# Kernel tuning notes

Hardware: AMD Instinct MI355X
Metric: run time of the kernel (lower is better)

The kernel has to match this reference:

```python
import jax, jax.numpy as jnp
import numpy as np

N = 50000          # nodes
E = 1250000        # edges (avg degree 25)
EMBED = 64
HIDS = [64, 64, 64]
EDGE_DIM = 7       # 1 + 6
VOCAB = 5 ** 8     # 390625
NEG_SLOPE = 0.01   # F.leaky_relu default


def setup_inputs() -> dict:
    key = jax.random.key(0)
    ks = jax.random.split(key, 14)
    L = len(HIDS)
    x = jax.random.randint(ks[0], (N,), 0, VOCAB)
    edge_index = jax.random.randint(ks[1], (2, E), 0, N)
    edge_attr = jax.random.normal(ks[2], (E, EDGE_DIM), dtype=jnp.float32)
    emb = jax.random.normal(ks[3], (VOCAB, EMBED), dtype=jnp.float32) * 0.02
    # all layers have in = out = 64, so params are stacked along layer axis
    lin1_w = jax.random.normal(ks[4], (L, EMBED + EDGE_DIM, HIDS[0]), dtype=jnp.float32) * 0.1
    att_l = jax.random.normal(ks[5], (L, HIDS[0]), dtype=jnp.float32) * 0.1
    att_r = jax.random.normal(ks[6], (L, EMBED), dtype=jnp.float32) * 0.1
    lin2_w = jax.random.normal(ks[7], (L, HIDS[0], HIDS[0]), dtype=jnp.float32) * 0.1
    gbias = jax.random.normal(ks[8], (L, HIDS[0]), dtype=jnp.float32) * 0.01
    d_cat = int(np.sum(HIDS)) + EMBED  # 256
    fc1_w = jax.random.normal(ks[9], (d_cat, 20), dtype=jnp.float32) * 0.05
    fc1_b = jax.random.normal(ks[10], (20,), dtype=jnp.float32) * 0.01
    fc2_w = jax.random.normal(ks[11], (20, 1), dtype=jnp.float32) * 0.1
    fc2_b = jax.random.normal(ks[12], (1,), dtype=jnp.float32) * 0.01
    return {"x": x, "edge_index": edge_index, "edge_attr": edge_attr, "emb": emb,
            "lin1_w": lin1_w, "att_l": att_l, "att_r": att_r, "lin2_w": lin2_w,
            "gbias": gbias, "fc1_w": fc1_w, "fc1_b": fc1_b, "fc2_w": fc2_w, "fc2_b": fc2_b}


def _gate_conv(h, src, dst, edge_attr, w1, al, ar, w2, b):
    # message from source j -> target i; attention softmax over edges sharing a target
    xj = jnp.concatenate([h[src], edge_attr], axis=-1)            # [E, in+7]
    xj = jax.nn.leaky_relu(xj @ w1, NEG_SLOPE)                    # [E, out]
    alpha = jax.nn.leaky_relu(jnp.sum(xj * al, -1) + jnp.sum(h[dst] * ar, -1), NEG_SLOPE)
    amax = jax.ops.segment_max(alpha, dst, num_segments=N)        # [N]
    ea = jnp.exp(alpha - amax[dst])                               # [E]
    denom = jax.ops.segment_sum(ea, dst, num_segments=N)          # [N]
    a = ea / (denom[dst] + 1e-16)
    msg = (xj @ w2) * a[:, None]                                  # [E, out]
    return jax.ops.segment_sum(msg, dst, num_segments=N) + b      # [N, out]


def reference(x, edge_index, edge_attr, emb, lin1_w, att_l, att_r, lin2_w,
              gbias, fc1_w, fc1_b, fc2_w, fc2_b):
    src, dst = edge_index[0], edge_index[1]
    h = emb[x]                                                    # [N, EMBED]
    feats = [h]
    for l in range(len(HIDS)):
        h = jax.nn.relu(_gate_conv(h, src, dst, edge_attr,
                                   lin1_w[l], att_l[l], att_r[l], lin2_w[l], gbias[l]))
        feats.append(h)
    hcat = jnp.concatenate(feats, axis=-1)                        # [N, 256]
    z = jax.nn.relu(hcat @ fc1_w + fc1_b)
    out = jax.nn.sigmoid(z @ fc2_w + fc2_b)
    return out.squeeze(-1)                                        # [N]
```

## Files before the change

kernel.cpp:

```cpp
#include <hip/hip_runtime.h>
#include <math.h>

#define NEG 0.01f

typedef _Float16 f16;
typedef f16 h2 __attribute__((ext_vector_type(2)));

__device__ __forceinline__ float lrelu(float x) { return x > 0.f ? x : NEG * x; }

__device__ __forceinline__ h2 lrelu2(h2 x) {
    h2 y = x * (f16)0.01f;
    return __builtin_elementwise_max(x, y);
}

__device__ __forceinline__ float q16_allsum(float v) {
    int x;
    x = __builtin_amdgcn_update_dpp(0, __float_as_int(v), 0xB1, 0xF, 0xF, true);  v += __int_as_float(x);
    x = __builtin_amdgcn_update_dpp(0, __float_as_int(v), 0x4E, 0xF, 0xF, true);  v += __int_as_float(x);
    x = __builtin_amdgcn_update_dpp(0, __float_as_int(v), 0x124, 0xF, 0xF, true); v += __int_as_float(x);
    x = __builtin_amdgcn_update_dpp(0, __float_as_int(v), 0x128, 0xF, 0xF, true); v += __int_as_float(x);
    return v;
}

__device__ __forceinline__ float x16_32_sum(float v) {
    v += __int_as_float(__builtin_amdgcn_ds_swizzle(__float_as_int(v), 0x401F));
    v += __shfl_xor(v, 32, 64);
    return v;
}

__global__ __launch_bounds__(256) void k_zero_gemm(
    int* __restrict__ deg, int N, int nz,
    const float* __restrict__ lin1, const float* __restrict__ attl,
    uint4* __restrict__ wpack,
    const int* __restrict__ x, const float* __restrict__ emb,
    const float* __restrict__ ar,
    f16* __restrict__ g, float* __restrict__ r_out, float* __restrict__ hcat)
{
    __shared__ __align__(16) float sA[64][68];
    __shared__ __align__(16) float sB[64 * 64];
    __shared__ float sar[64];
    int tid = threadIdx.x;
    if ((int)blockIdx.x < nz) {
        int i = blockIdx.x * 256 + tid;
        if (i < N) deg[i] = 0;
        if (i < 48) {
            int l = i >> 4, t = i & 15;
            const float* wb  = lin1 + (size_t)l * 71 * 64 + 64 * 64;
            const float* alp = attl + l * 64;
            unsigned int u[20];
#pragma unroll
            for (int j = 0; j < 4; j++) {
                int f = 4 * t + j;
                h2 a = { (f16)wb[f],       (f16)wb[64 + f]  }; u[j]      = __builtin_bit_cast(unsigned int, a);
                h2 b = { (f16)wb[128 + f], (f16)wb[192 + f] }; u[4 + j]  = __builtin_bit_cast(unsigned int, b);
                h2 c = { (f16)wb[256 + f], (f16)wb[320 + f] }; u[8 + j]  = __builtin_bit_cast(unsigned int, c);
                h2 d = { (f16)wb[384 + f], (f16)0.f         }; u[12 + j] = __builtin_bit_cast(unsigned int, d);
            }
            h2 e0 = { (f16)alp[4 * t],     (f16)alp[4 * t + 1] }; u[16] = __builtin_bit_cast(unsigned int, e0);
            h2 e1 = { (f16)alp[4 * t + 2], (f16)alp[4 * t + 3] }; u[17] = __builtin_bit_cast(unsigned int, e1);
            u[18] = 0; u[19] = 0;
            uint4* o = wpack + (size_t)i * 5;
            o[0] = make_uint4(u[0],  u[1],  u[2],  u[3]);
            o[1] = make_uint4(u[4],  u[5],  u[6],  u[7]);
            o[2] = make_uint4(u[8],  u[9],  u[10], u[11]);
            o[3] = make_uint4(u[12], u[13], u[14], u[15]);
            o[4] = make_uint4(u[16], u[17], u[18], u[19]);
        }
        return;
    }
    int row0 = ((int)blockIdx.x - nz) * 64;

    {
        const float4* b4 = (const float4*)lin1;
        float4* s4 = (float4*)sB;
        for (int i = tid; i < 1024; i += 256) s4[i] = b4[i];
    }
    if (tid < 64) sar[tid] = ar[tid];

#pragma unroll
    for (int pass = 0; pass < 4; ++pass) {
        int nl = pass * 16 + (tid & 15);
        int k4 = (tid >> 4) * 4;
        int n = row0 + nl; bool ok = n < N; if (!ok) n = N - 1;
        float4 v = *(const float4*)(emb + (size_t)x[n] * 64 + k4);
        sA[k4 + 0][nl] = v.x; sA[k4 + 1][nl] = v.y;
        sA[k4 + 2][nl] = v.z; sA[k4 + 3][nl] = v.w;
        if (ok) *(float4*)(hcat + (size_t)n * 256 + k4) = v;
    }
    __syncthreads();

    int tr = tid >> 4, tc = tid & 15;
    int r0 = tr * 4, c0 = tc * 4;
    float acc[4][4];
#pragma unroll
    for (int i = 0; i < 4; i++)
#pragma unroll
        for (int j = 0; j < 4; j++) acc[i][j] = 0.f;

#pragma unroll 4
    for (int k = 0; k < 64; ++k) {
        float4 b4 = *(const float4*)(sB + k * 64 + c0);
        float4 a0 = *(const float4*)&sA[k][r0];
#pragma unroll
        for (int j = 0; j < 4; j++) {
            float bj = (&b4.x)[j];
            acc[0][j] += a0.x * bj; acc[1][j] += a0.y * bj;
            acc[2][j] += a0.z * bj; acc[3][j] += a0.w * bj;
        }
    }

#pragma unroll
    for (int i = 0; i < 4; i++) {
        int n = row0 + r0 + i;
        if (n < N) {
            uint2 gw;
            gw.x = __builtin_bit_cast(unsigned int, __builtin_amdgcn_cvt_pkrtz(acc[i][0], acc[i][1]));
            gw.y = __builtin_bit_cast(unsigned int, __builtin_amdgcn_cvt_pkrtz(acc[i][2], acc[i][3]));
            *(uint2*)(g + (size_t)n * 64 + c0) = gw;
        }
    }
    if (tid < 64) {
        int n = row0 + tid;
        if (n < N) {
            float racc = 0.f;
#pragma unroll
            for (int k = 0; k < 64; k++) racc += sA[k][tid] * sar[k];
            r_out[n] = racc;
        }
    }
}

__global__ void k_count(const int* __restrict__ dst, int* __restrict__ deg,
                        int* __restrict__ rank, int E) {
    int e = blockIdx.x * blockDim.x + threadIdx.x;
    if (e < E) rank[e] = atomicAdd(&deg[dst[e]], 1);
}

__global__ __launch_bounds__(256) void k_scan_part(const int* __restrict__ deg,
                                                   int* __restrict__ bsum, int n) {
    __shared__ int sh[256];
    int b = blockIdx.x, t = threadIdx.x;
    int i0 = b * 1024 + t * 4;
    int s = 0;
    if (i0 + 3 < n) { int4 v = *(const int4*)(deg + i0); s = v.x + v.y + v.z + v.w; }
    else { for (int k = 0; k < 4; k++) if (i0 + k < n) s += deg[i0 + k]; }
    sh[t] = s; __syncthreads();
    for (int d = 128; d > 0; d >>= 1) { if (t < d) sh[t] += sh[t + d]; __syncthreads(); }
    if (t == 0) bsum[b] = sh[0];
}

__global__ __launch_bounds__(256) void k_scan_out(const int* __restrict__ deg,
                                                  const int* __restrict__ bsum,
                                                  int* __restrict__ off, int nb, int n) {
    __shared__ int sb[256];
    __shared__ int sh[256];
    int b = blockIdx.x, t = threadIdx.x;
    int v = (t < nb) ? bsum[t] : 0;
    sb[t] = v; __syncthreads();
    for (int d = 1; d < 256; d <<= 1) {
        int u = (t >= d) ? sb[t - d] : 0;
        __syncthreads(); sb[t] += u; __syncthreads();
    }
    int base = (b == 0) ? 0 : sb[b - 1];
    if (b == 0 && t == 0) off[n] = sb[255];
    int i0 = b * 1024 + t * 4;
    int4 v4 = make_int4(0, 0, 0, 0);
    if (i0 + 3 < n) v4 = *(const int4*)(deg + i0);
    else {
        v4.x = (i0     < n) ? deg[i0]     : 0;
        v4.y = (i0 + 1 < n) ? deg[i0 + 1] : 0;
        v4.z = (i0 + 2 < n) ? deg[i0 + 2] : 0;
        v4.w = (i0 + 3 < n) ? deg[i0 + 3] : 0;
    }
    int s = v4.x + v4.y + v4.z + v4.w;
    sh[t] = s; __syncthreads();
    for (int d = 1; d < 256; d <<= 1) {
        int u = (t >= d) ? sh[t - d] : 0;
        __syncthreads(); sh[t] += u; __syncthreads();
    }
    int ex = base + sh[t] - s;
    if (i0     < n) off[i0]     = ex;
    if (i0 + 1 < n) off[i0 + 1] = ex + v4.x;
    if (i0 + 2 < n) off[i0 + 2] = ex + v4.x + v4.y;
    if (i0 + 3 < n) off[i0 + 3] = ex + v4.x + v4.y + v4.z;
}

__global__ void k_fill(const int* __restrict__ src, const int* __restrict__ dst,
                       const float* __restrict__ eattr, const int* __restrict__ off,
                       const int* __restrict__ rank, uint4* __restrict__ rec, int E) {
    int e = blockIdx.x * 256 + threadIdx.x;
    if (e >= E) return;
    int slot = off[dst[e]] + rank[e];
    const float* ap = eattr + (size_t)e * 7;
    float a0 = ap[0], a1 = ap[1], a2 = ap[2], a3 = ap[3], a4 = ap[4], a5 = ap[5], a6 = ap[6];
    uint4 rv;
    h2 p01 = { (f16)a0, (f16)a1 };
    h2 p23 = { (f16)a2, (f16)a3 };
    h2 p45 = { (f16)a4, (f16)a5 };
    rv.x = __builtin_bit_cast(unsigned int, p01);
    rv.y = __builtin_bit_cast(unsigned int, p23);
    rv.z = __builtin_bit_cast(unsigned int, p45);
    unsigned int a6b = (unsigned int)__builtin_bit_cast(unsigned short, (f16)a6);
    rv.w = a6b | ((unsigned int)src[e] << 16);
    rec[slot] = rv;
}

__global__ __launch_bounds__(256) void k_gemm2g1(
    float* __restrict__ hc,
    const float* __restrict__ W2, const float* __restrict__ bias,
    const float* __restrict__ W1n, const float* __restrict__ arn,
    f16* __restrict__ g, float* __restrict__ r_out, int N)
{
    __shared__ __align__(16) float sA[64][68];
    __shared__ __align__(16) float sB[64 * 64];
    __shared__ float sar[64];
    int tid = threadIdx.x, row0 = blockIdx.x * 64;

    {
        const float4* b4 = (const float4*)W2;
        float4* s4 = (float4*)sB;
        for (int i = tid; i < 1024; i += 256) s4[i] = b4[i];
    }
    if (tid < 64) sar[tid] = arn[tid];

#pragma unroll
    for (int pass = 0; pass < 4; ++pass) {
        int nl = pass * 16 + (tid & 15);
        int k4 = (tid >> 4) * 4;
        int n = row0 + nl; if (n >= N) n = N - 1;
        float4 v = *(const float4*)(hc + (size_t)n * 256 + k4);
        sA[k4 + 0][nl] = v.x; sA[k4 + 1][nl] = v.y;
        sA[k4 + 2][nl] = v.z; sA[k4 + 3][nl] = v.w;
    }
    __syncthreads();

    int tr = tid >> 4, tc = tid & 15;
    int r0 = tr * 4, c0 = tc * 4;
    float acc[4][4];
#pragma unroll
    for (int i = 0; i < 4; i++)
#pragma unroll
        for (int j = 0; j < 4; j++) acc[i][j] = 0.f;

#pragma unroll 4
    for (int k = 0; k < 64; ++k) {
        float4 b4 = *(const float4*)(sB + k * 64 + c0);
        float4 a0 = *(const float4*)&sA[k][r0];
#pragma unroll
        for (int j = 0; j < 4; j++) {
            float bj = (&b4.x)[j];
            acc[0][j] += a0.x * bj; acc[1][j] += a0.y * bj;
            acc[2][j] += a0.z * bj; acc[3][j] += a0.w * bj;
        }
    }

    float4 bv = *(const float4*)(bias + c0);
#pragma unroll
    for (int i = 0; i < 4; i++) {
        acc[i][0] = fmaxf(acc[i][0] + bv.x, 0.f);
        acc[i][1] = fmaxf(acc[i][1] + bv.y, 0.f);
        acc[i][2] = fmaxf(acc[i][2] + bv.z, 0.f);
        acc[i][3] = fmaxf(acc[i][3] + bv.w, 0.f);
        int n = row0 + r0 + i;
        if (n < N) *(float4*)(hc + (size_t)n * 256 + c0) =
            make_float4(acc[i][0], acc[i][1], acc[i][2], acc[i][3]);
    }
    __syncthreads();

    {
        const float4* b4 = (const float4*)W1n;
        float4* s4 = (float4*)sB;
        for (int i = tid; i < 1024; i += 256) s4[i] = b4[i];
    }
#pragma unroll
    for (int i = 0; i < 4; i++)
#pragma unroll
        for (int j = 0; j < 4; j++) sA[c0 + j][r0 + i] = acc[i][j];
    __syncthreads();

#pragma unroll
    for (int i = 0; i < 4; i++)
#pragma unroll
        for (int j = 0; j < 4; j++) acc[i][j] = 0.f;

#pragma unroll 4
    for (int k = 0; k < 64; ++k) {
        float4 b4 = *(const float4*)(sB + k * 64 + c0);
        float4 a0 = *(const float4*)&sA[k][r0];
#pragma unroll
        for (int j = 0; j < 4; j++) {
            float bj = (&b4.x)[j];
            acc[0][j] += a0.x * bj; acc[1][j] += a0.y * bj;
            acc[2][j] += a0.z * bj; acc[3][j] += a0.w * bj;
        }
    }

#pragma unroll
    for (int i = 0; i < 4; i++) {
        int n = row0 + r0 + i;
        if (n < N) {
            uint2 gw;
            gw.x = __builtin_bit_cast(unsigned int, __builtin_amdgcn_cvt_pkrtz(acc[i][0], acc[i][1]));
            gw.y = __builtin_bit_cast(unsigned int, __builtin_amdgcn_cvt_pkrtz(acc[i][2], acc[i][3]));
            *(uint2*)(g + (size_t)n * 64 + c0) = gw;
        }
    }
    if (tid < 64) {
        int n = row0 + tid;
        if (n < N) {
            float racc = 0.f;
#pragma unroll
            for (int k = 0; k < 64; k++) racc += sA[k][tid] * sar[k];
            r_out[n] = racc;
        }
    }
}

struct ConvW {
    h2 w01[4], w23[4], w45[4], w6_[4];
    h2 al01, al23;
};

__device__ __forceinline__ void edge_math(uint4 rv, uint2 gv, bool valid, float ri,
                                          const ConvW& W, float4& s, float& den) {
    h2 a01 = __builtin_bit_cast(h2, rv.x);
    h2 a23 = __builtin_bit_cast(h2, rv.y);
    h2 a45 = __builtin_bit_cast(h2, rv.z);
    h2 a6p = __builtin_bit_cast(h2, rv.w & 0xFFFFu);
    h2 g01 = __builtin_bit_cast(h2, gv.x);
    h2 g23 = __builtin_bit_cast(h2, gv.y);

    float c0 = __builtin_amdgcn_fdot2(a01, W.w01[0],
               __builtin_amdgcn_fdot2(a23, W.w23[0],
               __builtin_amdgcn_fdot2(a45, W.w45[0],
               __builtin_amdgcn_fdot2(a6p, W.w6_[0], 0.f, false), false), false), false);
    float c1 = __builtin_amdgcn_fdot2(a01, W.w01[1],
               __builtin_amdgcn_fdot2(a23, W.w23[1],
               __builtin_amdgcn_fdot2(a45, W.w45[1],
               __builtin_amdgcn_fdot2(a6p, W.w6_[1], 0.f, false), false), false), false);
    float c2 = __builtin_amdgcn_fdot2(a01, W.w01[2],
               __builtin_amdgcn_fdot2(a23, W.w23[2],
               __builtin_amdgcn_fdot2(a45, W.w45[2],
               __builtin_amdgcn_fdot2(a6p, W.w6_[2], 0.f, false), false), false), false);
    float c3 = __builtin_amdgcn_fdot2(a01, W.w01[3],
               __builtin_amdgcn_fdot2(a23, W.w23[3],
               __builtin_amdgcn_fdot2(a45, W.w45[3],
               __builtin_amdgcn_fdot2(a6p, W.w6_[3], 0.f, false), false), false), false);

    h2 x01 = lrelu2(g01 + __builtin_amdgcn_cvt_pkrtz(c0, c1));
    h2 x23 = lrelu2(g23 + __builtin_amdgcn_cvt_pkrtz(c2, c3));
    float p = __builtin_amdgcn_fdot2(x01, W.al01,
              __builtin_amdgcn_fdot2(x23, W.al23, 0.f, false), false);
    p = q16_allsum(p);
    float alpha = lrelu(p + ri);
    float w = valid ? __expf(alpha) : 0.f;
    s.x += w * (float)x01.x; s.y += w * (float)x01.y;
    s.z += w * (float)x23.x; s.w += w * (float)x23.y;
    den += w;
}

__global__ __launch_bounds__(256) void k_conv(
    const int* __restrict__ off, const uint4* __restrict__ rec,
    const f16* __restrict__ g, const float* __restrict__ r,
    const uint4* __restrict__ wpack, float* __restrict__ aggdst, int N)
{
    int lane = threadIdx.x & 63;
    int wid  = threadIdx.x >> 6;
    int node = blockIdx.x * 4 + wid;
    if (node >= N) return;
    int q = lane >> 4, l16 = lane & 15;

    ConvW W;
    {
        const uint4* wp = wpack + l16 * 5;
        uint4 v0 = wp[0], v1 = wp[1], v2 = wp[2], v3 = wp[3], v4 = wp[4];
        W.w01[0] = __builtin_bit_cast(h2, v0.x); W.w01[1] = __builtin_bit_cast(h2, v0.y);
        W.w01[2] = __builtin_bit_cast(h2, v0.z); W.w01[3] = __builtin_bit_cast(h2, v0.w);
        W.w23[0] = __builtin_bit_cast(h2, v1.x); W.w23[1] = __builtin_bit_cast(h2, v1.y);
        W.w23[2] = __builtin_bit_cast(h2, v1.z); W.w23[3] = __builtin_bit_cast(h2, v1.w);
        W.w45[0] = __builtin_bit_cast(h2, v2.x); W.w45[1] = __builtin_bit_cast(h2, v2.y);
        W.w45[2] = __builtin_bit_cast(h2, v2.z); W.w45[3] = __builtin_bit_cast(h2, v2.w);
        W.w6_[0] = __builtin_bit_cast(h2, v3.x); W.w6_[1] = __builtin_bit_cast(h2, v3.y);
        W.w6_[2] = __builtin_bit_cast(h2, v3.z); W.w6_[3] = __builtin_bit_cast(h2, v3.w);
        W.al01   = __builtin_bit_cast(h2, v4.x); W.al23   = __builtin_bit_cast(h2, v4.y);
    }

    float ri = r[node];
    int e0 = off[node], e1 = off[node + 1];
    int goff = 4 * l16;

    float4 s = make_float4(0.f, 0.f, 0.f, 0.f);
    float den = 0.f;
    if (e0 < e1) {
        int last = e1 - 1;
        int b0 = e0 + q;
        uint4 ra = rec[b0      < e1 ? b0      : last];
        uint4 rb = rec[b0 + 4  < e1 ? b0 + 4  : last];
        uint4 rc = rec[b0 + 8  < e1 ? b0 + 8  : last];
        uint4 rd = rec[b0 + 12 < e1 ? b0 + 12 : last];
        uint2 ga = *(const uint2*)(g + (size_t)(ra.w >> 16) * 64 + goff);
        uint2 gb = *(const uint2*)(g + (size_t)(rb.w >> 16) * 64 + goff);
        uint2 gc = *(const uint2*)(g + (size_t)(rc.w >> 16) * 64 + goff);
        uint2 gd = *(const uint2*)(g + (size_t)(rd.w >> 16) * 64 + goff);
        int b1 = b0 + 16;
        uint4 na = rec[b1      < e1 ? b1      : last];
        uint4 nb = rec[b1 + 4  < e1 ? b1 + 4  : last];
        uint4 nc = rec[b1 + 8  < e1 ? b1 + 8  : last];
        uint4 nd = rec[b1 + 12 < e1 ? b1 + 12 : last];
        for (int e = e0; e < e1; e += 16) {
            uint2 gna = *(const uint2*)(g + (size_t)(na.w >> 16) * 64 + goff);
            uint2 gnb = *(const uint2*)(g + (size_t)(nb.w >> 16) * 64 + goff);
            uint2 gnc = *(const uint2*)(g + (size_t)(nc.w >> 16) * 64 + goff);
            uint2 gnd = *(const uint2*)(g + (size_t)(nd.w >> 16) * 64 + goff);
            int b2 = e + 32 + q;
            uint4 ma = rec[b2      < e1 ? b2      : last];
            uint4 mb = rec[b2 + 4  < e1 ? b2 + 4  : last];
            uint4 mc = rec[b2 + 8  < e1 ? b2 + 8  : last];
            uint4 md = rec[b2 + 12 < e1 ? b2 + 12 : last];
            bool va = (e + q)      < e1, vb = (e + 4 + q)  < e1;
            bool vc = (e + 8 + q)  < e1, vd = (e + 12 + q) < e1;
            edge_math(ra, ga, va, ri, W, s, den);
            edge_math(rb, gb, vb, ri, W, s, den);
            edge_math(rc, gc, vc, ri, W, s, den);
            edge_math(rd, gd, vd, ri, W, s, den);
            ra = na; rb = nb; rc = nc; rd = nd;
            ga = gna; gb = gnb; gc = gnc; gd = gnd;
            na = ma; nb = mb; nc = mc; nd = md;
        }
    }
    s.x = x16_32_sum(s.x); s.y = x16_32_sum(s.y);
    s.z = x16_32_sum(s.z); s.w = x16_32_sum(s.w);
    den = x16_32_sum(den);
    float inv = 1.f / (den + 1e-16f);
    if (q == 0) {
        float4 o = make_float4(s.x * inv, s.y * inv, s.z * inv, s.w * inv);
        *(float4*)(aggdst + (size_t)node * 256 + goff) = o;
    }
}

__global__ __launch_bounds__(256) void k_gemm2head(
    const float* __restrict__ hcat,
    const float* __restrict__ W2, const float* __restrict__ bias,
    const float* __restrict__ f1w, const float* __restrict__ f1b,
    const float* __restrict__ f2w, const float* __restrict__ f2b,
    float* __restrict__ out, int N)
{
    __shared__ __align__(16) float sA[64][132];
    __shared__ __align__(16) float sBW[5120];
    __shared__ float sP[128 * 20];
    int tid = threadIdx.x, row0 = blockIdx.x * 128;

    {
        const float4* b4 = (const float4*)W2;
        float4* s4 = (float4*)sBW;
        for (int i = tid; i < 1024; i += 256) s4[i] = b4[i];
    }
#pragma unroll
    for (int pass = 0; pass < 8; ++pass) {
        int nl = pass * 16 + (tid & 15);
        int k4 = (tid >> 4) * 4;
        int n = row0 + nl; if (n >= N) n = N - 1;
        float4 v = *(const float4*)(hcat + (size_t)n * 256 + 192 + k4);
        sA[k4 + 0][nl] = v.x; sA[k4 + 1][nl] = v.y;
        sA[k4 + 2][nl] = v.z; sA[k4 + 3][nl] = v.w;
    }
    __syncthreads();

    int tr = tid >> 4, tc = tid & 15;
    int r0 = tr * 8, c0 = tc * 4;
    float acc[8][4];
#pragma unroll
    for (int i = 0; i < 8; i++)
#pragma unroll
        for (int j = 0; j < 4; j++) acc[i][j] = 0.f;

#pragma unroll 4
    for (int k = 0; k < 64; ++k) {
        float4 b4 = *(const float4*)(sBW + k * 64 + c0);
        float4 a0 = *(const float4*)&sA[k][r0];
        float4 a1 = *(const float4*)&sA[k][r0 + 4];
#pragma unroll
        for (int j = 0; j < 4; j++) {
            float bj = (&b4.x)[j];
            acc[0][j] += a0.x * bj; acc[1][j] += a0.y * bj;
            acc[2][j] += a0.z * bj; acc[3][j] += a0.w * bj;
            acc[4][j] += a1.x * bj; acc[5][j] += a1.y * bj;
            acc[6][j] += a1.z * bj; acc[7][j] += a1.w * bj;
        }
    }

    float4 fw[5];
    {
        const float4* w4 = (const float4*)f1w;
#pragma unroll
        for (int i2 = 0; i2 < 5; i2++) fw[i2] = w4[tid + i2 * 256];
    }
    __syncthreads();

    float* sO = &sA[0][0];
    float4 bv = *(const float4*)(bias + c0);
#pragma unroll
    for (int i = 0; i < 8; i++) {
        acc[i][0] = fmaxf(acc[i][0] + bv.x, 0.f);
        acc[i][1] = fmaxf(acc[i][1] + bv.y, 0.f);
        acc[i][2] = fmaxf(acc[i][2] + bv.z, 0.f);
        acc[i][3] = fmaxf(acc[i][3] + bv.w, 0.f);
        int rr = r0 + i;
        sO[rr * 65 + c0 + 0] = acc[i][0];
        sO[rr * 65 + c0 + 1] = acc[i][1];
        sO[rr * 65 + c0 + 2] = acc[i][2];
        sO[rr * 65 + c0 + 3] = acc[i][3];
    }
    {
        float4* sw4 = (float4*)sBW;
#pragma unroll
        for (int i2 = 0; i2 < 5; i2++) sw4[tid + i2 * 256] = fw[i2];
    }
    __syncthreads();

    int rloc = tid & 127;
    int half = tid >> 7;
    int n = row0 + rloc;
    int nn = (n < N) ? n : N - 1;
    float z[20];
#pragma unroll
    for (int j = 0; j < 20; j++) z[j] = 0.f;
    const float4* hr = (const float4*)(hcat + (size_t)nn * 256);
    if (half == 0) {
        for (int k4 = 0; k4 < 32; k4++) {
            float4 h = hr[k4];
            const float* wr = sBW + k4 * 80;
#pragma unroll
            for (int j = 0; j < 20; j++)
                z[j] += h.x * wr[j] + h.y * wr[20 + j] + h.z * wr[40 + j] + h.w * wr[60 + j];
        }
    } else {
        for (int k4 = 32; k4 < 48; k4++) {
            float4 h = hr[k4];
            const float* wr = sBW + k4 * 80;
#pragma unroll
            for (int j = 0; j < 20; j++)
                z[j] += h.x * wr[j] + h.y * wr[20 + j] + h.z * wr[40 + j] + h.w * wr[60 + j];
        }
        for (int k = 0; k < 64; k += 2) {
            float hx = sO[rloc * 65 + k], hy = sO[rloc * 65 + k + 1];
            const float* wr = sBW + (192 + k) * 20;
#pragma unroll
            for (int j = 0; j < 20; j++)
                z[j] += hx * wr[j] + hy * wr[20 + j];
        }
#pragma unroll
        for (int j = 0; j < 20; j++) sP[rloc * 20 + j] = z[j];
    }
    __syncthreads();
    if (half == 0 && n < N) {
        float o = f2b[0];
#pragma unroll
        for (int j = 0; j < 20; j++) {
            float zj = z[j] + sP[rloc * 20 + j] + f1b[j];
            o += fmaxf(zj, 0.f) * f2w[j];
        }
        out[n] = 1.f / (1.f + __expf(-o));
    }
}

extern "C" void kernel_launch(void* const* d_in, const int* in_sizes, int n_in,
                              void* d_out, int out_size, void* d_ws, size_t ws_size,
                              hipStream_t stream) {
    const int*   x     = (const int*)d_in[0];
    const int*   eidx  = (const int*)d_in[1];
    const float* eattr = (const float*)d_in[2];
    const float* emb   = (const float*)d_in[3];
    const float* lin1  = (const float*)d_in[4];
    const float* attl  = (const float*)d_in[5];
    const float* attr_ = (const float*)d_in[6];
    const float* lin2  = (const float*)d_in[7];
    const float* gbias = (const float*)d_in[8];
    const float* f1w   = (const float*)d_in[9];
    const float* f1b   = (const float*)d_in[10];
    const float* f2w   = (const float*)d_in[11];
    const float* f2b   = (const float*)d_in[12];
    float* out = (float*)d_out;

    int N = in_sizes[0];
    int E = in_sizes[1] / 2;
    const int* src = eidx;
    const int* dst = eidx + E;

    char* p = (char*)d_ws;
    auto alloc = [&](size_t bytes) { void* q = (void*)p; p += (bytes + 255) & ~(size_t)255; return q; };
    float* hcat = (float*)alloc((size_t)N * 256 * 4);
    f16*   g    = (f16*)alloc((size_t)N * 64 * 2);
    float* r    = (float*)alloc((size_t)N * 4);
    int*   off  = (int*)alloc((size_t)(N + 1) * 4);
    int*   deg  = (int*)alloc((size_t)N * 4);
    int*   rank = (int*)alloc((size_t)E * 4);
    int*   bsum = (int*)alloc(256 * 4);
    uint4* rec  = (uint4*)alloc((size_t)E * 16);
    uint4* wpack = (uint4*)alloc((size_t)48 * 5 * 16);

    int nz    = (N + 255) / 256;
    int nbs   = (N + 1023) / 1024;
    int nbE   = (E + 255) / 256;
    int nbg64 = (N + 63) / 64;
    int nbg128 = (N + 127) / 128;
    int nbc   = (N + 3) / 4;

    k_zero_gemm<<<nz + nbg64, 256, 0, stream>>>(deg, N, nz, lin1, attl, wpack,
                                                x, emb, attr_, g, r, hcat);
    k_count<<<nbE, 256, 0, stream>>>(dst, deg, rank, E);
    k_scan_part<<<nbs, 256, 0, stream>>>(deg, bsum, N);
    k_scan_out<<<nbs, 256, 0, stream>>>(deg, bsum, off, nbs, N);
    k_fill<<<nbE, 256, 0, stream>>>(src, dst, eattr, off, rank, rec, E);

    k_conv<<<nbc, 256, 0, stream>>>(off, rec, g, r, wpack, hcat + 64, N);
    for (int l = 0; l < 2; l++) {
        k_gemm2g1<<<nbg64, 256, 0, stream>>>(hcat + 64 * (l + 1),
                                             lin2 + (size_t)l * 4096, gbias + l * 64,
                                             lin1 + (size_t)(l + 1) * 71 * 64,
                                             attr_ + (l + 1) * 64, g, r, N);
        k_conv<<<nbc, 256, 0, stream>>>(off, rec, g, r,
                                        wpack + (size_t)(l + 1) * 80,
                                        hcat + 64 * (l + 2), N);
    }
    k_gemm2head<<<nbg128, 256, 0, stream>>>(hcat, lin2 + 2 * 4096, gbias + 128,
                                            f1w, f1b, f2w, f2b, out, N);
}
```

Before: 509.9 us.

## Fuse degree count into first GEMM, pad edge records, shuffle-reduce head

Several changes land together. The degree zeroing and weight packing move into a small pre-kernel that also zero-pads 64 extra edge records. Edge counting is fused with the layer-0 embedding GEMM in one launch, with 4 edges per thread and the GEMM tile shrunk to 32 rows. With the padding, the conv loop drops its per-load clamping of record indices. The fill kernel handles two edges per thread, and the head kernel replaces its shared-memory partial-sum exchange and barrier with a lane shuffle. Together these aim to cut launch count, index arithmetic and synchronisation, at the cost of reading padded zero records whose source index 0 must be valid.

```diff
diff --git a/kernel.cpp b/kernel.cpp
--- a/kernel.cpp
+++ b/kernel.cpp
@@ -28,47 +28,65 @@
     return v;
 }
 
-__global__ __launch_bounds__(256) void k_zero_gemm(
-    int* __restrict__ deg, int N, int nz,
-    const float* __restrict__ lin1, const float* __restrict__ attl,
-    uint4* __restrict__ wpack,
+__global__ void k_pre(int* __restrict__ deg, int N,
+                      const float* __restrict__ lin1, const float* __restrict__ attl,
+                      uint4* __restrict__ wpack, uint4* __restrict__ rec, int E) {
+    int i = blockIdx.x * blockDim.x + threadIdx.x;
+    if (i < N) deg[i] = 0;
+    if (i < 48) {
+        int l = i >> 4, t = i & 15;
+        const float* wb  = lin1 + (size_t)l * 71 * 64 + 64 * 64;
+        const float* alp = attl + l * 64;
+        unsigned int u[20];
+#pragma unroll
+        for (int j = 0; j < 4; j++) {
+            int f = 4 * t + j;
+            h2 a = { (f16)wb[f],       (f16)wb[64 + f]  }; u[j]      = __builtin_bit_cast(unsigned int, a);
+            h2 b = { (f16)wb[128 + f], (f16)wb[192 + f] }; u[4 + j]  = __builtin_bit_cast(unsigned int, b);
+            h2 c = { (f16)wb[256 + f], (f16)wb[320 + f] }; u[8 + j]  = __builtin_bit_cast(unsigned int, c);
+            h2 d = { (f16)wb[384 + f], (f16)0.f         }; u[12 + j] = __builtin_bit_cast(unsigned int, d);
+        }
+        h2 e0 = { (f16)alp[4 * t],     (f16)alp[4 * t + 1] }; u[16] = __builtin_bit_cast(unsigned int, e0);
+        h2 e1 = { (f16)alp[4 * t + 2], (f16)alp[4 * t + 3] }; u[17] = __builtin_bit_cast(unsigned int, e1);
+        u[18] = 0; u[19] = 0;
+        uint4* o = wpack + (size_t)i * 5;
+        o[0] = make_uint4(u[0],  u[1],  u[2],  u[3]);
+        o[1] = make_uint4(u[4],  u[5],  u[6],  u[7]);
+        o[2] = make_uint4(u[8],  u[9],  u[10], u[11]);
+        o[3] = make_uint4(u[12], u[13], u[14], u[15]);
+        o[4] = make_uint4(u[16], u[17], u[18], u[19]);
+    } else if (i >= 48 && i < 112) {
+        rec[E + i - 48] = make_uint4(0, 0, 0, 0);
+    }
+}
+
+__global__ __launch_bounds__(256) void k_count_gemm0(
+    const int* __restrict__ dst, int* __restrict__ deg, int* __restrict__ rank,
+    int E, int nbC,
     const int* __restrict__ x, const float* __restrict__ emb,
-    const float* __restrict__ ar,
-    f16* __restrict__ g, float* __restrict__ r_out, float* __restrict__ hcat)
+    const float* __restrict__ lin1, const float* __restrict__ ar,
+    f16* __restrict__ g, float* __restrict__ r_out, float* __restrict__ hcat, int N)
 {
-    __shared__ __align__(16) float sA[64][68];
+    __shared__ __align__(16) float sA[64][36];
     __shared__ __align__(16) float sB[64 * 64];
     __shared__ float sar[64];
     int tid = threadIdx.x;
-    if ((int)blockIdx.x < nz) {
-        int i = blockIdx.x * 256 + tid;
-        if (i < N) deg[i] = 0;
-        if (i < 48) {
-            int l = i >> 4, t = i & 15;
-            const float* wb  = lin1 + (size_t)l * 71 * 64 + 64 * 64;
-            const float* alp = attl + l * 64;
-            unsigned int u[20];
-#pragma unroll
-            for (int j = 0; j < 4; j++) {
-                int f = 4 * t + j;
-                h2 a = { (f16)wb[f],       (f16)wb[64 + f]  }; u[j]      = __builtin_bit_cast(unsigned int, a);
-                h2 b = { (f16)wb[128 + f], (f16)wb[192 + f] }; u[4 + j]  = __builtin_bit_cast(unsigned int, b);
-                h2 c = { (f16)wb[256 + f], (f16)wb[320 + f] }; u[8 + j]  = __builtin_bit_cast(unsigned int, c);
-                h2 d = { (f16)wb[384 + f], (f16)0.f         }; u[12 + j] = __builtin_bit_cast(unsigned int, d);
-            }
-            h2 e0 = { (f16)alp[4 * t],     (f16)alp[4 * t + 1] }; u[16] = __builtin_bit_cast(unsigned int, e0);
-            h2 e1 = { (f16)alp[4 * t + 2], (f16)alp[4 * t + 3] }; u[17] = __builtin_bit_cast(unsigned int, e1);
-            u[18] = 0; u[19] = 0;
-            uint4* o = wpack + (size_t)i * 5;
-            o[0] = make_uint4(u[0],  u[1],  u[2],  u[3]);
-            o[1] = make_uint4(u[4],  u[5],  u[6],  u[7]);
-            o[2] = make_uint4(u[8],  u[9],  u[10], u[11]);
-            o[3] = make_uint4(u[12], u[13], u[14], u[15]);
-            o[4] = make_uint4(u[16], u[17], u[18], u[19]);
+    if ((int)blockIdx.x < nbC) {
+        int e = (blockIdx.x * 256 + tid) * 4;
+        if (e + 3 < E) {
+            int4 d = *(const int4*)(dst + e);
+            int r0 = atomicAdd(&deg[d.x], 1);
+            int r1 = atomicAdd(&deg[d.y], 1);
+            int r2 = atomicAdd(&deg[d.z], 1);
+            int r3 = atomicAdd(&deg[d.w], 1);
+            *(int4*)(rank + e) = make_int4(r0, r1, r2, r3);
+        } else {
+            for (int k = 0; k < 4; k++)
+                if (e + k < E) rank[e + k] = atomicAdd(&deg[dst[e + k]], 1);
         }
         return;
     }
-    int row0 = ((int)blockIdx.x - nz) * 64;
+    int row0 = ((int)blockIdx.x - nbC) * 32;
 
     {
         const float4* b4 = (const float4*)lin1;
@@ -78,7 +96,7 @@
     if (tid < 64) sar[tid] = ar[tid];
 
 #pragma unroll
-    for (int pass = 0; pass < 4; ++pass) {
+    for (int pass = 0; pass < 2; ++pass) {
         int nl = pass * 16 + (tid & 15);
         int k4 = (tid >> 4) * 4;
         int n = row0 + nl; bool ok = n < N; if (!ok) n = N - 1;
@@ -90,27 +108,26 @@
     __syncthreads();
 
     int tr = tid >> 4, tc = tid & 15;
-    int r0 = tr * 4, c0 = tc * 4;
-    float acc[4][4];
-#pragma unroll
-    for (int i = 0; i < 4; i++)
+    int r0 = tr * 2, c0 = tc * 4;
+    float acc[2][4];
+#pragma unroll
+    for (int i = 0; i < 2; i++)
 #pragma unroll
         for (int j = 0; j < 4; j++) acc[i][j] = 0.f;
 
 #pragma unroll 4
     for (int k = 0; k < 64; ++k) {
         float4 b4 = *(const float4*)(sB + k * 64 + c0);
-        float4 a0 = *(const float4*)&sA[k][r0];
+        float2 a0 = *(const float2*)&sA[k][r0];
 #pragma unroll
         for (int j = 0; j < 4; j++) {
             float bj = (&b4.x)[j];
             acc[0][j] += a0.x * bj; acc[1][j] += a0.y * bj;
-            acc[2][j] += a0.z * bj; acc[3][j] += a0.w * bj;
-        }
-    }
-
-#pragma unroll
-    for (int i = 0; i < 4; i++) {
+        }
+    }
+
+#pragma unroll
+    for (int i = 0; i < 2; i++) {
         int n = row0 + r0 + i;
         if (n < N) {
             uint2 gw;
@@ -119,7 +136,7 @@
             *(uint2*)(g + (size_t)n * 64 + c0) = gw;
         }
     }
-    if (tid < 64) {
+    if (tid < 32) {
         int n = row0 + tid;
         if (n < N) {
             float racc = 0.f;
@@ -128,12 +145,6 @@
             r_out[n] = racc;
         }
     }
-}
-
-__global__ void k_count(const int* __restrict__ dst, int* __restrict__ deg,
-                        int* __restrict__ rank, int E) {
-    int e = blockIdx.x * blockDim.x + threadIdx.x;
-    if (e < E) rank[e] = atomicAdd(&deg[dst[e]], 1);
 }
 
 __global__ __launch_bounds__(256) void k_scan_part(const int* __restrict__ deg,
@@ -188,21 +199,27 @@
 __global__ void k_fill(const int* __restrict__ src, const int* __restrict__ dst,
                        const float* __restrict__ eattr, const int* __restrict__ off,
                        const int* __restrict__ rank, uint4* __restrict__ rec, int E) {
-    int e = blockIdx.x * 256 + threadIdx.x;
+    int e = (blockIdx.x * 256 + threadIdx.x) * 2;
     if (e >= E) return;
-    int slot = off[dst[e]] + rank[e];
-    const float* ap = eattr + (size_t)e * 7;
-    float a0 = ap[0], a1 = ap[1], a2 = ap[2], a3 = ap[3], a4 = ap[4], a5 = ap[5], a6 = ap[6];
-    uint4 rv;
-    h2 p01 = { (f16)a0, (f16)a1 };
-    h2 p23 = { (f16)a2, (f16)a3 };
-    h2 p45 = { (f16)a4, (f16)a5 };
-    rv.x = __builtin_bit_cast(unsigned int, p01);
-    rv.y = __builtin_bit_cast(unsigned int, p23);
-    rv.z = __builtin_bit_cast(unsigned int, p45);
-    unsigned int a6b = (unsigned int)__builtin_bit_cast(unsigned short, (f16)a6);
-    rv.w = a6b | ((unsigned int)src[e] << 16);
-    rec[slot] = rv;
+    bool two = (e + 1 < E);
+#pragma unroll
+    for (int k = 0; k < 2; k++) {
+        if (k == 1 && !two) break;
+        int ee = e + k;
+        int slot = off[dst[ee]] + rank[ee];
+        const float* ap = eattr + (size_t)ee * 7;
+        float a0 = ap[0], a1 = ap[1], a2 = ap[2], a3 = ap[3], a4 = ap[4], a5 = ap[5], a6 = ap[6];
+        uint4 rv;
+        h2 p01 = { (f16)a0, (f16)a1 };
+        h2 p23 = { (f16)a2, (f16)a3 };
+        h2 p45 = { (f16)a4, (f16)a5 };
+        rv.x = __builtin_bit_cast(unsigned int, p01);
+        rv.y = __builtin_bit_cast(unsigned int, p23);
+        rv.z = __builtin_bit_cast(unsigned int, p45);
+        unsigned int a6b = (unsigned int)__builtin_bit_cast(unsigned short, (f16)a6);
+        rv.w = a6b | ((unsigned int)src[ee] << 16);
+        rec[slot] = rv;
+    }
 }
 
 __global__ __launch_bounds__(256) void k_gemm2g1(
@@ -387,36 +404,25 @@
 
     float ri = r[node];
     int e0 = off[node], e1 = off[node + 1];
-    int goff = 4 * l16;
+    const f16* gq = g + 4 * l16;
 
     float4 s = make_float4(0.f, 0.f, 0.f, 0.f);
     float den = 0.f;
     if (e0 < e1) {
-        int last = e1 - 1;
-        int b0 = e0 + q;
-        uint4 ra = rec[b0      < e1 ? b0      : last];
-        uint4 rb = rec[b0 + 4  < e1 ? b0 + 4  : last];
-        uint4 rc = rec[b0 + 8  < e1 ? b0 + 8  : last];
-        uint4 rd = rec[b0 + 12 < e1 ? b0 + 12 : last];
-        uint2 ga = *(const uint2*)(g + (size_t)(ra.w >> 16) * 64 + goff);
-        uint2 gb = *(const uint2*)(g + (size_t)(rb.w >> 16) * 64 + goff);
-        uint2 gc = *(const uint2*)(g + (size_t)(rc.w >> 16) * 64 + goff);
-        uint2 gd = *(const uint2*)(g + (size_t)(rd.w >> 16) * 64 + goff);
-        int b1 = b0 + 16;
-        uint4 na = rec[b1      < e1 ? b1      : last];
-        uint4 nb = rec[b1 + 4  < e1 ? b1 + 4  : last];
-        uint4 nc = rec[b1 + 8  < e1 ? b1 + 8  : last];
-        uint4 nd = rec[b1 + 12 < e1 ? b1 + 12 : last];
+        const uint4* rp = rec + e0 + q;
+        uint4 ra = rp[0], rb = rp[4], rc = rp[8], rd = rp[12];
+        uint2 ga = *(const uint2*)(gq + (size_t)(ra.w >> 16) * 64);
+        uint2 gb = *(const uint2*)(gq + (size_t)(rb.w >> 16) * 64);
+        uint2 gc = *(const uint2*)(gq + (size_t)(rc.w >> 16) * 64);
+        uint2 gd = *(const uint2*)(gq + (size_t)(rd.w >> 16) * 64);
+        uint4 na = rp[16], nb = rp[20], nc = rp[24], nd = rp[28];
         for (int e = e0; e < e1; e += 16) {
-            uint2 gna = *(const uint2*)(g + (size_t)(na.w >> 16) * 64 + goff);
-            uint2 gnb = *(const uint2*)(g + (size_t)(nb.w >> 16) * 64 + goff);
-            uint2 gnc = *(const uint2*)(g + (size_t)(nc.w >> 16) * 64 + goff);
-            uint2 gnd = *(const uint2*)(g + (size_t)(nd.w >> 16) * 64 + goff);
-            int b2 = e + 32 + q;
-            uint4 ma = rec[b2      < e1 ? b2      : last];
-            uint4 mb = rec[b2 + 4  < e1 ? b2 + 4  : last];
-            uint4 mc = rec[b2 + 8  < e1 ? b2 + 8  : last];
-            uint4 md = rec[b2 + 12 < e1 ? b2 + 12 : last];
+            uint2 gna = *(const uint2*)(gq + (size_t)(na.w >> 16) * 64);
+            uint2 gnb = *(const uint2*)(gq + (size_t)(nb.w >> 16) * 64);
+            uint2 gnc = *(const uint2*)(gq + (size_t)(nc.w >> 16) * 64);
+            uint2 gnd = *(const uint2*)(gq + (size_t)(nd.w >> 16) * 64);
+            rp += 16;
+            uint4 ma = rp[16], mb = rp[20], mc = rp[24], md = rp[28];
             bool va = (e + q)      < e1, vb = (e + 4 + q)  < e1;
             bool vc = (e + 8 + q)  < e1, vd = (e + 12 + q) < e1;
             edge_math(ra, ga, va, ri, W, s, den);
@@ -434,7 +440,7 @@
     float inv = 1.f / (den + 1e-16f);
     if (q == 0) {
         float4 o = make_float4(s.x * inv, s.y * inv, s.z * inv, s.w * inv);
-        *(float4*)(aggdst + (size_t)node * 256 + goff) = o;
+        *(float4*)(aggdst + (size_t)node * 256 + 4 * l16) = o;
     }
 }
 
@@ -445,9 +451,8 @@
     const float* __restrict__ f2w, const float* __restrict__ f2b,
     float* __restrict__ out, int N)
 {
-    __shared__ __align__(16) float sA[64][132];
+    __shared__ __align__(16) float sA[64][130];
     __shared__ __align__(16) float sBW[5120];
-    __shared__ float sP[128 * 20];
     int tid = threadIdx.x, row0 = blockIdx.x * 128;
 
     {
@@ -518,8 +523,8 @@
     }
     __syncthreads();
 
-    int rloc = tid & 127;
-    int half = tid >> 7;
+    int rloc = tid >> 1;
+    int half = tid & 1;
     int n = row0 + rloc;
     int nn = (n < N) ? n : N - 1;
     float z[20];
@@ -549,15 +554,14 @@
             for (int j = 0; j < 20; j++)
                 z[j] += hx * wr[j] + hy * wr[20 + j];
         }
-#pragma unroll
-        for (int j = 0; j < 20; j++) sP[rloc * 20 + j] = z[j];
-    }
-    __syncthreads();
+    }
+#pragma unroll
+    for (int j = 0; j < 20; j++) z[j] += __shfl_xor(z[j], 1, 64);
     if (half == 0 && n < N) {
         float o = f2b[0];
 #pragma unroll
         for (int j = 0; j < 20; j++) {
-            float zj = z[j] + sP[rloc * 20 + j] + f1b[j];
+            float zj = z[j] + f1b[j];
             o += fmaxf(zj, 0.f) * f2w[j];
         }
         out[n] = 1.f / (1.f + __expf(-o));
@@ -596,22 +600,23 @@
     int*   deg  = (int*)alloc((size_t)N * 4);
     int*   rank = (int*)alloc((size_t)E * 4);
     int*   bsum = (int*)alloc(256 * 4);
-    uint4* rec  = (uint4*)alloc((size_t)E * 16);
+    uint4* rec  = (uint4*)alloc((size_t)(E + 64) * 16);
     uint4* wpack = (uint4*)alloc((size_t)48 * 5 * 16);
 
-    int nz    = (N + 255) / 256;
     int nbs   = (N + 1023) / 1024;
-    int nbE   = (E + 255) / 256;
+    int nbC   = ((E + 3) / 4 + 255) / 256;
+    int nbG0  = (N + 31) / 32;
+    int nbF   = ((E + 1) / 2 + 255) / 256;
     int nbg64 = (N + 63) / 64;
     int nbg128 = (N + 127) / 128;
     int nbc   = (N + 3) / 4;
 
-    k_zero_gemm<<<nz + nbg64, 256, 0, stream>>>(deg, N, nz, lin1, attl, wpack,
-                                                x, emb, attr_, g, r, hcat);
-    k_count<<<nbE, 256, 0, stream>>>(dst, deg, rank, E);
+    k_pre<<<(N + 255) / 256, 256, 0, stream>>>(deg, N, lin1, attl, wpack, rec, E);
+    k_count_gemm0<<<nbC + nbG0, 256, 0, stream>>>(dst, deg, rank, E, nbC,
+                                                  x, emb, lin1, attr_, g, r, hcat, N);
     k_scan_part<<<nbs, 256, 0, stream>>>(deg, bsum, N);
     k_scan_out<<<nbs, 256, 0, stream>>>(deg, bsum, off, nbs, N);
-    k_fill<<<nbE, 256, 0, stream>>>(src, dst, eattr, off, rank, rec, E);
+    k_fill<<<nbF, 256, 0, stream>>>(src, dst, eattr, off, rank, rec, E);
 
     k_conv<<<nbc, 256, 0, stream>>>(off, rec, g, r, wpack, hcat + 64, N);
     for (int l = 0; l < 2; l++) {
```

Measured after the change: 514.0 us. About the same (+0.8%).
